# Kernel optimization log

Measured on AMD Instinct MI355X. Metric: run time of the kernel, lower is better.

The kernel has to match this reference:

```python
import jax, jax.numpy as jnp
import numpy as np
import math

L, E, H, F, V, ML, B, S = 6, 1024, 16, 4096, 1024, 1024, 4, 1024
PAD = V - 1


def setup_inputs() -> dict:
    key = jax.random.key(0)
    ks = jax.random.split(key, 16)
    sc = 0.02
    nrm = lambda k, sh: jax.random.normal(k, sh, jnp.float32) * sc
    return dict(
        sequences=jax.random.randint(ks[0], (B, S), 0, V - 1),
        embed=nrm(ks[1], (V, E)),
        pos_emb=nrm(ks[2], (1, ML + 2, E)),
        dist_emb=nrm(ks[3], (ML + 1, H)),
        in_w=nrm(ks[4], (L, 3 * E, E)), in_b=nrm(ks[5], (L, 3 * E)),
        out_w=nrm(ks[6], (L, E, E)), out_b=nrm(ks[7], (L, E)),
        ln1_g=jnp.ones((L, E)), ln1_b=jnp.zeros((L, E)),
        ff1_w=nrm(ks[8], (L, F, E)), ff1_b=nrm(ks[9], (L, F)),
        ff2_w=nrm(ks[10], (L, E, F)), ff2_b=nrm(ks[11], (L, E)),
        ln2_g=jnp.ones((L, E)), ln2_b=jnp.zeros((L, E)),
        lnf_g=jnp.ones((E,)), lnf_b=jnp.zeros((E,)),
        gen_w=nrm(ks[12], (V, E)), gen_b=jnp.zeros((V,)),
    )


def _layer_norm(h, g, b, eps=1e-5):
    m = h.mean(-1, keepdims=True)
    v = ((h - m) ** 2).mean(-1, keepdims=True)
    return (h - m) * jax.lax.rsqrt(v + eps) * g + b


def reference(sequences, embed, pos_emb, dist_emb, in_w, in_b, out_w, out_b,
              ln1_g, ln1_b, ff1_w, ff1_b, ff2_w, ff2_b, ln2_g, ln2_b,
              lnf_g, lnf_b, gen_w, gen_b):
    b_, s_ = sequences.shape
    dh = E // H
    # token embedding * sqrt(E) + learned positional embedding
    x = embed[sequences] * math.sqrt(E) + pos_emb[:, :s_]  # [B,S,E]
    # relative-distance attention bias, clamped at max_len
    idx = jnp.arange(s_)
    dist = jnp.minimum(jnp.abs(idx[None, :] - idx[:, None]), ML)  # [S,S]
    bias = dist_emb[dist].transpose(2, 0, 1)[None]  # [1,H,S,S]
    causal = idx[None, :] <= idx[:, None]  # lower-triangular allowed
    bias = jnp.where(causal[None, None], bias, -jnp.inf)
    # key padding mask (additive -inf on padded keys)
    kpm = (sequences == PAD)  # [B,S]
    bias = jnp.where(kpm[:, None, None, :], -jnp.inf, bias)  # [B,H,S,S]

    scale = 1.0 / math.sqrt(dh)
    for l in range(L):
        qkv = jnp.einsum('bse,fe->bsf', x, in_w[l]) + in_b[l]
        q, k, v = jnp.split(qkv, 3, axis=-1)
        q = q.reshape(b_, s_, H, dh).transpose(0, 2, 1, 3)
        k = k.reshape(b_, s_, H, dh).transpose(0, 2, 1, 3)
        v = v.reshape(b_, s_, H, dh).transpose(0, 2, 1, 3)
        scores = jnp.einsum('bhqd,bhkd->bhqk', q, k) * scale + bias
        att = jax.nn.softmax(scores, axis=-1)
        ctx = jnp.einsum('bhqk,bhkd->bhqd', att, v)
        ctx = ctx.transpose(0, 2, 1, 3).reshape(b_, s_, E)
        attn_out = jnp.einsum('bse,fe->bsf', ctx, out_w[l]) + out_b[l]
        x = _layer_norm(x + attn_out, ln1_g[l], ln1_b[l])  # post-norm
        h = jax.nn.gelu(jnp.einsum('bse,fe->bsf', x, ff1_w[l]) + ff1_b[l], approximate=False)
        h = jnp.einsum('bsf,ef->bse', h, ff2_w[l]) + ff2_b[l]
        x = _layer_norm(x + h, ln2_g[l], ln2_b[l])
    x = _layer_norm(x, lnf_g, lnf_b)  # final encoder norm
    logits = jnp.einsum('bse,ve->bsv', x, gen_w) + gen_b
    return logits
```

## Files before the change

### kernel.cpp

```cpp
#include <hip/hip_runtime.h>
#include <math.h>
#include <stdint.h>

constexpr int kL = 6;
constexpr int kE = 1024;
constexpr int kH = 16;
constexpr int kF = 4096;
constexpr int kV = 1024;
constexpr int kB = 4;
constexpr int kS = 1024;
constexpr int kRows = kB * kS;

typedef __bf16 bf16_t;
typedef __bf16 bf16x8 __attribute__((ext_vector_type(8)));
typedef __bf16 bf16x4 __attribute__((ext_vector_type(4)));
typedef float f32x4 __attribute__((ext_vector_type(4)));
typedef unsigned int u32x2 __attribute__((ext_vector_type(2)));

#define AS1 __attribute__((address_space(1)))
#define AS3 __attribute__((address_space(3)))

__device__ __forceinline__ void gload_lds16(const void* g, void* l) {
  __builtin_amdgcn_global_load_lds((const AS1 unsigned int*)g, (AS3 unsigned int*)l, 16, 0, 0);
}

__device__ __forceinline__ unsigned lds_u32(const void* p) {
  return (unsigned)(uintptr_t)p;
}

__device__ __forceinline__ float gelu_f(float x) {
  return 0.5f * x * (1.0f + erff(x * 0.70710678118654752440f));
}

template <int CTRL>
__device__ __forceinline__ float dppf(float v) {
  return __builtin_bit_cast(float, __builtin_amdgcn_update_dpp(
      __builtin_bit_cast(int, v), __builtin_bit_cast(int, v), CTRL, 0xF, 0xF, false));
}

__global__ void cast_kernel(const float* __restrict__ in, bf16_t* __restrict__ out, int n4) {
  const int stride = gridDim.x * blockDim.x;
  for (int i = blockIdx.x * blockDim.x + threadIdx.x; i < n4; i += stride) {
    const float4 v = *(const float4*)(in + (size_t)i * 4);
    bf16x4 o;
    o[0] = (bf16_t)v.x; o[1] = (bf16_t)v.y; o[2] = (bf16_t)v.z; o[3] = (bf16_t)v.w;
    *(bf16x4*)(out + (size_t)i * 4) = o;
  }
}

__global__ void embed_kernel(const int* __restrict__ seq, const float* __restrict__ emb,
                             const float* __restrict__ pos, float* __restrict__ x32,
                             bf16_t* __restrict__ xb) {
  const int r = blockIdx.x;
  const int s = r & 1023;
  const int tok = seq[r];
  const int c = threadIdx.x << 2;
  const float4 e = *(const float4*)(emb + (size_t)tok * kE + c);
  const float4 pz = *(const float4*)(pos + (size_t)s * kE + c);
  float4 v;
  v.x = e.x * 32.0f + pz.x;
  v.y = e.y * 32.0f + pz.y;
  v.z = e.z * 32.0f + pz.z;
  v.w = e.w * 32.0f + pz.w;
  *(float4*)(x32 + (size_t)r * kE + c) = v;
  bf16x4 o;
  o[0] = (bf16_t)v.x; o[1] = (bf16_t)v.y; o[2] = (bf16_t)v.z; o[3] = (bf16_t)v.w;
  *(bf16x4*)(xb + (size_t)r * kE + c) = o;
}

template <int MODE>
__global__ void addln_kernel(float* __restrict__ x32, const void* __restrict__ res,
                             const float* __restrict__ gg, const float* __restrict__ bb,
                             bf16_t* __restrict__ xb, const float* __restrict__ bias2) {
  __shared__ float red[8];
  const int r = blockIdx.x;
  const int c = threadIdx.x << 2;
  float4 v = *(const float4*)(x32 + (size_t)r * kE + c);
  if (MODE == 0) {
    const bf16x4 t = *(const bf16x4*)((const bf16_t*)res + (size_t)r * kE + c);
    v.x += (float)t[0]; v.y += (float)t[1]; v.z += (float)t[2]; v.w += (float)t[3];
  }
  if (MODE == 2) {
    const bf16_t* p = (const bf16_t*)res;
#pragma unroll
    for (int part = 0; part < 4; ++part) {
      const bf16x4 t = *(const bf16x4*)(p + (size_t)part * kRows * kE + (size_t)r * kE + c);
      v.x += (float)t[0]; v.y += (float)t[1]; v.z += (float)t[2]; v.w += (float)t[3];
    }
    const float4 b2 = *(const float4*)(bias2 + c);
    v.x += b2.x; v.y += b2.y; v.z += b2.z; v.w += b2.w;
  }
  float s = v.x + v.y + v.z + v.w;
  float q = v.x * v.x + v.y * v.y + v.z * v.z + v.w * v.w;
#pragma unroll
  for (int off = 32; off >= 1; off >>= 1) {
    s += __shfl_xor(s, off, 64);
    q += __shfl_xor(q, off, 64);
  }
  const int w = threadIdx.x >> 6, lane = threadIdx.x & 63;
  if (lane == 0) { red[w] = s; red[4 + w] = q; }
  __syncthreads();
  s = red[0] + red[1] + red[2] + red[3];
  q = red[4] + red[5] + red[6] + red[7];
  const float mean = s * (1.0f / 1024.0f);
  const float var = q * (1.0f / 1024.0f) - mean * mean;
  const float rstd = rsqrtf(var + 1e-5f);
  const float4 g4 = *(const float4*)(gg + c);
  const float4 b4 = *(const float4*)(bb + c);
  float4 o;
  o.x = (v.x - mean) * rstd * g4.x + b4.x;
  o.y = (v.y - mean) * rstd * g4.y + b4.y;
  o.z = (v.z - mean) * rstd * g4.z + b4.z;
  o.w = (v.w - mean) * rstd * g4.w + b4.w;
  if (MODE != 1) *(float4*)(x32 + (size_t)r * kE + c) = o;
  bf16x4 ob;
  ob[0] = (bf16_t)o.x; ob[1] = (bf16_t)o.y; ob[2] = (bf16_t)o.z; ob[3] = (bf16_t)o.w;
  *(bf16x4*)(xb + (size_t)r * kE + c) = ob;
}

template <int EPI>
__launch_bounds__(256, 3)
__global__ void gemm_bt_kernel(const bf16_t* __restrict__ A, const bf16_t* __restrict__ Bt,
                               const float* __restrict__ bias, void* __restrict__ Cv,
                               int M, int N, int K) {
  __shared__ bf16_t lA[128 * 32];
  __shared__ bf16_t lB[128 * 32];
  const int tid = threadIdx.x;
  const int w = tid >> 6;
  const int lane = tid & 63;
  const int g = lane >> 4;
  const int lr = lane & 15;
  const int bm0 = blockIdx.y << 7;
  const int bn0 = blockIdx.x << 7;
  const int wm = (w >> 1) << 6;
  const int wn = (w & 1) << 6;

  const int sr = lane >> 2;
  const int sc = (lane & 3) << 4;

  const char* srcA0 = (const char*)(A + (size_t)(bm0 + (w << 5) + sr) * K) + sc;
  const char* srcA1 = (const char*)(A + (size_t)(bm0 + (w << 5) + 16 + sr) * K) + sc;
  const char* srcB0 = (const char*)(Bt + (size_t)(bn0 + (w << 5) + sr) * K) + sc;
  const char* srcB1 = (const char*)(Bt + (size_t)(bn0 + (w << 5) + 16 + sr) * K) + sc;
  bf16_t* dA0 = lA + (size_t)(w << 5) * 32;
  bf16_t* dA1 = lA + (size_t)((w << 5) + 16) * 32;
  bf16_t* dB0 = lB + (size_t)(w << 5) * 32;
  bf16_t* dB1 = lB + (size_t)((w << 5) + 16) * 32;

  f32x4 zz = {0.f, 0.f, 0.f, 0.f};
  f32x4 acc[4][4];
#pragma unroll
  for (int i = 0; i < 4; ++i)
#pragma unroll
    for (int j = 0; j < 4; ++j) acc[i][j] = zz;

  const bf16_t* pa[4];
  const bf16_t* pb[4];
#pragma unroll
  for (int i = 0; i < 4; ++i) {
    pa[i] = lA + (size_t)(wm + i * 16 + lr) * 32 + g * 8;
    pb[i] = lB + (size_t)(wn + i * 16 + lr) * 32 + g * 8;
  }

  const int NT = K >> 5;
  for (int t = 0; t < NT; ++t) {
    gload_lds16(srcA0, dA0);
    gload_lds16(srcA1, dA1);
    gload_lds16(srcB0, dB0);
    gload_lds16(srcB1, dB1);
    srcA0 += 64; srcA1 += 64; srcB0 += 64; srcB1 += 64;
    __syncthreads();
    bf16x8 a[4], b[4];
#pragma unroll
    for (int i = 0; i < 4; ++i) a[i] = *(const bf16x8*)pa[i];
#pragma unroll
    for (int i = 0; i < 4; ++i) b[i] = *(const bf16x8*)pb[i];
#pragma unroll
    for (int i = 0; i < 4; ++i)
#pragma unroll
      for (int j = 0; j < 4; ++j)
        acc[i][j] = __builtin_amdgcn_mfma_f32_16x16x32_bf16(a[i], b[j], acc[i][j], 0, 0, 0);
    __syncthreads();
  }

#pragma unroll
  for (int i = 0; i < 4; ++i) {
#pragma unroll
    for (int j = 0; j < 4; ++j) {
      const int col = bn0 + wn + j * 16 + lr;
      const float bv = bias[col];
#pragma unroll
      for (int rg = 0; rg < 4; ++rg) {
        const int row = bm0 + wm + i * 16 + g * 4 + rg;
        float v = acc[i][j][rg] + bv;
        if (EPI == 1) {
          ((float*)Cv)[(size_t)row * N + col] = v;
        } else {
          ((bf16_t*)Cv)[(size_t)row * N + col] = (bf16_t)v;
        }
      }
    }
  }
}

template <int EPI>
__launch_bounds__(512, 2)
__global__ void gemm256_kernel(const bf16_t* __restrict__ A, const bf16_t* __restrict__ Bt,
                               const float* __restrict__ bias, void* __restrict__ Cv,
                               int ldA, int ldB, int ldC, int kc, size_t zstride) {
  __shared__ bf16_t lA[2][256 * 64];
  __shared__ bf16_t lB[2][256 * 64];
  const int tid = threadIdx.x;
  const int w = tid >> 6, lane = tid & 63, g = lane >> 4, lr = lane & 15;

  const int nwg = gridDim.x * gridDim.y;
  const int lin = blockIdx.y * gridDim.x + blockIdx.x;
  const int cpx = nwg >> 3;
  const int swz = (lin & 7) * cpx + (lin >> 3);
  const int bx = swz % gridDim.x, by = swz / gridDim.x;
  const int bm0 = by << 8, bn0 = bx << 8;
  const int wr = w >> 2, wc = w & 3;
  const int wm = wr << 7, wn = wc << 6;
  const int k0 = blockIdx.z * kc;

  const int lrow = lane >> 3, lcol8 = lane & 7;
  const int scol = ((lcol8 ^ lrow) << 3);
  const bf16_t* pA = A + (size_t)(bm0 + lrow) * ldA + k0 + scol;
  const bf16_t* pB = Bt + (size_t)(bn0 + lrow) * ldB + k0 + scol;

  const int ra1_0 = w * 8,                        ra1_1 = 128 + w * 8;
  const int ra4_0 = 64 + w * 8,                   ra4_1 = 192 + w * 8;
  const int rb2_0 = (w >> 2) * 64 + (w & 3) * 8,  rb2_1 = rb2_0 + 128;
  const int rb3_0 = rb2_0 + 32,                   rb3_1 = rb2_1 + 32;

#define STG_A(bufi, t, rb) gload_lds16(pA + (size_t)(rb) * ldA + (t) * 64, &lA[bufi][(rb) * 64])
#define STG_B(bufi, t, rb) gload_lds16(pB + (size_t)(rb) * ldB + (t) * 64, &lB[bufi][(rb) * 64])
#define STAGE_R1(bufi, t) { STG_A(bufi, t, ra1_0); STG_A(bufi, t, ra1_1); }
#define STAGE_R2(bufi, t) { STG_B(bufi, t, rb2_0); STG_B(bufi, t, rb2_1); }
#define STAGE_R3(bufi, t) { STG_B(bufi, t, rb3_0); STG_B(bufi, t, rb3_1); }
#define STAGE_R4(bufi, t) { STG_A(bufi, t, ra4_0); STG_A(bufi, t, ra4_1); }

  const int cs0 = (g * 8) ^ ((lr & 7) << 3);
  const int cs1 = (32 + g * 8) ^ ((lr & 7) << 3);
#define LDA8(bufi, row, cs) (*(const bf16x8*)&lA[bufi][(row) * 64 + (cs)])
#define LDB8(bufi, row, cs) (*(const bf16x8*)&lB[bufi][(row) * 64 + (cs)])

#define PH_MID()                                          \
  __builtin_amdgcn_sched_barrier(0);                      \
  __builtin_amdgcn_s_barrier();                           \
  asm volatile("s_waitcnt lgkmcnt(0)" ::: "memory");      \
  __builtin_amdgcn_sched_barrier(0);                      \
  __builtin_amdgcn_s_setprio(1)

#define PH_END()                                          \
  __builtin_amdgcn_s_setprio(0);                          \
  __builtin_amdgcn_sched_barrier(0);                      \
  __builtin_amdgcn_s_barrier();                           \
  __builtin_amdgcn_sched_barrier(0)

#define PH_END_VM()                                       \
  __builtin_amdgcn_s_setprio(0);                          \
  __builtin_amdgcn_sched_barrier(0);                      \
  asm volatile("s_waitcnt vmcnt(6)" ::: "memory");        \
  __builtin_amdgcn_s_barrier();                           \
  __builtin_amdgcn_sched_barrier(0)

  f32x4 zz = {0.f, 0.f, 0.f, 0.f};
  f32x4 acc[8][4];
#pragma unroll
  for (int i = 0; i < 8; ++i)
#pragma unroll
    for (int j = 0; j < 4; ++j) acc[i][j] = zz;

  const int NT = kc >> 6;

  STAGE_R1(0, 0); STAGE_R2(0, 0); STAGE_R3(0, 0); STAGE_R4(0, 0);
  STAGE_R1(1, 1); STAGE_R2(1, 1); STAGE_R3(1, 1);
  asm volatile("s_waitcnt vmcnt(6)" ::: "memory");
  __builtin_amdgcn_s_barrier();
  __builtin_amdgcn_sched_barrier(0);

  bf16x8 a0[4][2], a1[4][2], b[4][2];

  for (int t = 0; t < NT; ++t) {
    const int bz = t & 1;
#pragma unroll
    for (int i = 0; i < 4; ++i) {
      a0[i][0] = LDA8(bz, wm + i * 16 + lr, cs0);
      a0[i][1] = LDA8(bz, wm + i * 16 + lr, cs1);
    }
#pragma unroll
    for (int j = 0; j < 2; ++j) {
      b[j][0] = LDB8(bz, wn + j * 16 + lr, cs0);
      b[j][1] = LDB8(bz, wn + j * 16 + lr, cs1);
    }
    if (t + 1 < NT) STAGE_R4(bz ^ 1, t + 1);
    PH_MID();
#pragma unroll
    for (int i = 0; i < 4; ++i)
#pragma unroll
      for (int j = 0; j < 2; ++j) {
        acc[i][j] = __builtin_amdgcn_mfma_f32_16x16x32_bf16(a0[i][0], b[j][0], acc[i][j], 0, 0, 0);
        acc[i][j] = __builtin_amdgcn_mfma_f32_16x16x32_bf16(a0[i][1], b[j][1], acc[i][j], 0, 0, 0);
      }
    PH_END();
#pragma unroll
    for (int j = 2; j < 4; ++j) {
      b[j][0] = LDB8(bz, wn + j * 16 + lr, cs0);
      b[j][1] = LDB8(bz, wn + j * 16 + lr, cs1);
    }
    if (t + 2 < NT) STAGE_R1(bz, t + 2);
    PH_MID();
#pragma unroll
    for (int i = 0; i < 4; ++i)
#pragma unroll
      for (int j = 2; j < 4; ++j) {
        acc[i][j] = __builtin_amdgcn_mfma_f32_16x16x32_bf16(a0[i][0], b[j][0], acc[i][j], 0, 0, 0);
        acc[i][j] = __builtin_amdgcn_mfma_f32_16x16x32_bf16(a0[i][1], b[j][1], acc[i][j], 0, 0, 0);
      }
    PH_END();
#pragma unroll
    for (int i = 0; i < 4; ++i) {
      a1[i][0] = LDA8(bz, wm + 64 + i * 16 + lr, cs0);
      a1[i][1] = LDA8(bz, wm + 64 + i * 16 + lr, cs1);
    }
    if (t + 2 < NT) STAGE_R2(bz, t + 2);
    PH_MID();
#pragma unroll
    for (int i = 0; i < 4; ++i)
#pragma unroll
      for (int j = 0; j < 2; ++j) {
        acc[4 + i][j] = __builtin_amdgcn_mfma_f32_16x16x32_bf16(a1[i][0], b[j][0], acc[4 + i][j], 0, 0, 0);
        acc[4 + i][j] = __builtin_amdgcn_mfma_f32_16x16x32_bf16(a1[i][1], b[j][1], acc[4 + i][j], 0, 0, 0);
      }
    PH_END();
    if (t + 2 < NT) STAGE_R3(bz, t + 2);
    PH_MID();
#pragma unroll
    for (int i = 0; i < 4; ++i)
#pragma unroll
      for (int j = 2; j < 4; ++j) {
        acc[4 + i][j] = __builtin_amdgcn_mfma_f32_16x16x32_bf16(a1[i][0], b[j][0], acc[4 + i][j], 0, 0, 0);
        acc[4 + i][j] = __builtin_amdgcn_mfma_f32_16x16x32_bf16(a1[i][1], b[j][1], acc[4 + i][j], 0, 0, 0);
      }
    PH_END_VM();
  }

  bf16_t* outb = (bf16_t*)Cv;
  if (EPI == 3) outb += (size_t)blockIdx.z * zstride;
#pragma unroll
  for (int i = 0; i < 8; ++i) {
#pragma unroll
    for (int j = 0; j < 4; ++j) {
      const int col = bn0 + wn + j * 16 + lr;
      float bv = 0.0f;
      if (EPI != 3) bv = bias[col];
#pragma unroll
      for (int rg = 0; rg < 4; ++rg) {
        const int row = bm0 + wm + i * 16 + g * 4 + rg;
        float v = acc[i][j][rg] + bv;
        if (EPI == 2) v = gelu_f(v);
        outb[(size_t)row * ldC + col] = (bf16_t)v;
      }
    }
  }
#undef STG_A
#undef STG_B
#undef STAGE_R1
#undef STAGE_R2
#undef STAGE_R3
#undef STAGE_R4
#undef LDA8
#undef LDB8
#undef PH_MID
#undef PH_END
#undef PH_END_VM
}

__launch_bounds__(256, 3)
__global__ void attn_kernel(const bf16_t* __restrict__ qkv, const int* __restrict__ seq,
                            const float* __restrict__ dist_emb, bf16_t* __restrict__ ctx) {
  __shared__ float sbias[1024];
  __shared__ unsigned char spad[1024];
  __shared__ bf16_t kbuf[2][64 * 64];
  __shared__ bf16_t vbuf[2][4096];
  __shared__ bf16_t pbuf[4][16][72];
  const int tid = threadIdx.x;
  const int w = tid >> 6, lane = tid & 63, g = lane >> 4, lr = lane & 15;
  const int bid = blockIdx.x;
  const int qt = 15 - (bid >> 6);
  const int h = bid & 15, b = (bid >> 4) & 3;

  const int q0 = qt * 64 + w * 16;
  const bf16_t* qp = qkv + ((size_t)(b * kS + q0 + lr)) * 3072 + h * 64;

  const int p = (w * 64 + lane) * 16;
  const int s_kv = ((p >> 11) << 4) + ((p >> 5) & 15);
  const int s_dv = (((p >> 9) & 3) << 4) + ((p & 31) >> 1);
  const bf16_t* vsrc0 = qkv + ((size_t)(b * kS + s_kv)) * 3072 + 2048 + h * 64 + s_dv;

  const int klrow = (w << 3) + (lane >> 3);
  const int kscol = ((lane & 7) ^ (lane >> 3)) << 3;
  const bf16_t* ksrc0 = qkv + ((size_t)(b * kS + klrow)) * 3072 + 1024 + h * 64 + kscol;

  const int cs0k = (g ^ (lr & 7)) << 3;
  const int cs1k = ((4 + g) ^ (lr & 7)) << 3;

  const int* seqb = seq + b * kS;
  const int nt = qt + 1;

#define STAGEKV(bufi, kt_) {                                                        \
    gload_lds16(ksrc0 + (size_t)((kt_) * 64) * 3072, &kbuf[bufi][(w << 3) * 64]);   \
    gload_lds16(ksrc0 + (size_t)((kt_) * 64 + 32) * 3072,                           \
                &kbuf[bufi][(32 + (w << 3)) * 64]);                                 \
    gload_lds16(vsrc0 + (size_t)((kt_) * 64) * 3072, &vbuf[bufi][w << 9]);          \
    gload_lds16(vsrc0 + (size_t)((kt_) * 64 + 32) * 3072,                           \
                &vbuf[bufi][2048 + (w << 9)]);                                      \
  }

  STAGEKV(0, 0);
  const bf16x8 qf0 = *(const bf16x8*)(qp + g * 8);
  const bf16x8 qf1 = *(const bf16x8*)(qp + 32 + g * 8);
  for (int i = tid; i < 1024; i += 256) {
    sbias[i] = dist_emb[i * kH + h];
    spad[i] = (seqb[i] == kV - 1) ? 1 : 0;
  }

  f32x4 zz = {0.f, 0.f, 0.f, 0.f};
  f32x4 oacc[4];
#pragma unroll
  for (int n = 0; n < 4; ++n) oacc[n] = zz;
  float m_[4], l_[4];
#pragma unroll
  for (int j = 0; j < 4; ++j) { m_[j] = -1e30f; l_[j] = 0.f; }

  __syncthreads();

#define ATT_STEP64(kt_, bz) do {                                                    \
    bf16x8 kf0[4], kf1[4];                                                          \
    _Pragma("unroll")                                                               \
    for (int ns = 0; ns < 4; ++ns) {                                                \
      const int krow = (ns * 16 + lr) * 64;                                         \
      kf0[ns] = *(const bf16x8*)&kbuf[bz][krow + cs0k];                             \
      kf1[ns] = *(const bf16x8*)&kbuf[bz][krow + cs1k];                             \
    }                                                                               \
    f32x4 s_[4];                                                                    \
    _Pragma("unroll")                                                               \
    for (int ns = 0; ns < 4; ++ns) {                                                \
      f32x4 z = zz;                                                                 \
      z = __builtin_amdgcn_mfma_f32_16x16x32_bf16(qf0, kf0[ns], z, 0, 0, 0);        \
      z = __builtin_amdgcn_mfma_f32_16x16x32_bf16(qf1, kf1[ns], z, 0, 0, 0);        \
      s_[ns] = z;                                                                   \
    }                                                                               \
    const int colb = (kt_) * 64 + lr;                                               \
    bool pad[4];                                                                    \
    _Pragma("unroll")                                                               \
    for (int ns = 0; ns < 4; ++ns) pad[ns] = spad[colb + ns * 16] != 0;             \
    float sv[4][4], mj[4];                                                          \
    _Pragma("unroll")                                                               \
    for (int j = 0; j < 4; ++j) {                                                   \
      const int r = q0 + g * 4 + j;                                                 \
      _Pragma("unroll")                                                             \
      for (int ns = 0; ns < 4; ++ns) {                                              \
        const int cc = colb + ns * 16;                                              \
        sv[ns][j] = (cc <= r && !pad[ns]) ? s_[ns][j] * 0.125f + sbias[r - cc]      \
                                          : -1e30f;                                 \
      }                                                                             \
      mj[j] = fmaxf(fmaxf(sv[0][j], sv[1][j]), fmaxf(sv[2][j], sv[3][j]));          \
      mj[j] = fmaxf(mj[j], dppf<0x121>(mj[j]));                                     \
      mj[j] = fmaxf(mj[j], dppf<0x122>(mj[j]));                                     \
      mj[j] = fmaxf(mj[j], dppf<0x124>(mj[j]));                                     \
      mj[j] = fmaxf(mj[j], dppf<0x128>(mj[j]));                                     \
    }                                                                               \
    float corr[4], pv[4][4];                                                        \
    _Pragma("unroll")                                                               \
    for (int j = 0; j < 4; ++j) {                                                   \
      const float mn = fmaxf(m_[j], mj[j]);                                         \
      corr[j] = __expf(m_[j] - mn);                                                 \
      m_[j] = mn;                                                                   \
      _Pragma("unroll")                                                             \
      for (int ns = 0; ns < 4; ++ns) pv[ns][j] = __expf(sv[ns][j] - mn);            \
      float rs = (pv[0][j] + pv[1][j]) + (pv[2][j] + pv[3][j]);                     \
      rs += dppf<0x121>(rs);                                                        \
      rs += dppf<0x122>(rs);                                                        \
      rs += dppf<0x124>(rs);                                                        \
      rs += dppf<0x128>(rs);                                                        \
      l_[j] = l_[j] * corr[j] + rs;                                                 \
    }                                                                               \
    _Pragma("unroll")                                                               \
    for (int n = 0; n < 4; ++n) {                                                   \
      f32x4 t = oacc[n];                                                            \
      t[0] *= corr[0]; t[1] *= corr[1]; t[2] *= corr[2]; t[3] *= corr[3];           \
      oacc[n] = t;                                                                  \
    }                                                                               \
    _Pragma("unroll")                                                               \
    for (int j = 0; j < 4; ++j) {                                                   \
      _Pragma("unroll")                                                             \
      for (int ns = 0; ns < 4; ++ns)                                                \
        pbuf[w][g * 4 + j][ns * 16 + lr] = (bf16_t)pv[ns][j];                       \
    }                                                                               \
    asm volatile("s_waitcnt lgkmcnt(0)" ::: "memory");                              \
    const bf16x4 pa0 = *(const bf16x4*)&pbuf[w][lr][g * 4];                         \
    const bf16x4 pa1 = *(const bf16x4*)&pbuf[w][lr][16 + g * 4];                    \
    const bf16x4 pa2 = *(const bf16x4*)&pbuf[w][lr][32 + g * 4];                    \
    const bf16x4 pa3 = *(const bf16x4*)&pbuf[w][lr][48 + g * 4];                    \
    bf16x8 pfl, pfh;                                                                \
    _Pragma("unroll")                                                               \
    for (int j = 0; j < 4; ++j) {                                                   \
      pfl[j] = pa0[j]; pfl[4 + j] = pa1[j];                                         \
      pfh[j] = pa2[j]; pfh[4 + j] = pa3[j];                                         \
    }                                                                               \
    const unsigned vb0 = lds_u32(&vbuf[bz][0]) + g * 128 + lr * 8;                  \
    u32x2 vt[8], vth[8];                                                            \
    _Pragma("unroll")                                                               \
    for (int n = 0; n < 4; ++n) {                                                   \
      asm volatile("ds_read_b64_tr_b16 %0, %2\n\t"                                  \
                   "ds_read_b64_tr_b16 %1, %2 offset:2048"                          \
                   : "=&v"(vt[n * 2]), "=&v"(vt[n * 2 + 1])                         \
                   : "v"(vb0 + n * 512)                                             \
                   : "memory");                                                     \
      asm volatile("ds_read_b64_tr_b16 %0, %2 offset:4096\n\t"                      \
                   "ds_read_b64_tr_b16 %1, %2 offset:6144"                          \
                   : "=&v"(vth[n * 2]), "=&v"(vth[n * 2 + 1])                       \
                   : "v"(vb0 + n * 512)                                             \
                   : "memory");                                                     \
    }                                                                               \
    asm volatile("s_waitcnt lgkmcnt(0)" ::: "memory");                              \
    __builtin_amdgcn_sched_barrier(0);                                              \
    _Pragma("unroll")                                                               \
    for (int n = 0; n < 4; ++n) {                                                   \
      const bf16x4 v0 = __builtin_bit_cast(bf16x4, vt[n * 2]);                      \
      const bf16x4 v1 = __builtin_bit_cast(bf16x4, vt[n * 2 + 1]);                  \
      bf16x8 vf;                                                                    \
      _Pragma("unroll")                                                             \
      for (int j = 0; j < 4; ++j) { vf[j] = v0[j]; vf[4 + j] = v1[j]; }             \
      oacc[n] = __builtin_amdgcn_mfma_f32_16x16x32_bf16(pfl, vf, oacc[n], 0, 0, 0); \
      const bf16x4 h0 = __builtin_bit_cast(bf16x4, vth[n * 2]);                     \
      const bf16x4 h1 = __builtin_bit_cast(bf16x4, vth[n * 2 + 1]);                 \
      bf16x8 vfh;                                                                   \
      _Pragma("unroll")                                                             \
      for (int j = 0; j < 4; ++j) { vfh[j] = h0[j]; vfh[4 + j] = h1[j]; }           \
      oacc[n] = __builtin_amdgcn_mfma_f32_16x16x32_bf16(pfh, vfh, oacc[n], 0, 0, 0);\
    }                                                                               \
  } while (0)

  for (int kt = 0; kt < nt; kt += 2) {
    if (kt + 1 < nt) STAGEKV(1, kt + 1);
    ATT_STEP64(kt, 0);
    __syncthreads();
    if (kt + 2 < nt) STAGEKV(0, kt + 2);
    if (kt + 1 < nt) ATT_STEP64(kt + 1, 1);
    __syncthreads();
  }
#undef ATT_STEP64
#undef STAGEKV

#pragma unroll
  for (int j = 0; j < 4; ++j) {
    const float inv = 1.0f / l_[j];
    const int r = q0 + g * 4 + j;
    bf16_t* dst = ctx + ((size_t)(b * kS + r)) * kE + h * 64;
#pragma unroll
    for (int n = 0; n < 4; ++n) dst[n * 16 + lr] = (bf16_t)(oacc[n][j] * inv);
  }
}

extern "C" void kernel_launch(void* const* d_in, const int* in_sizes, int n_in,
                              void* d_out, int out_size, void* d_ws, size_t ws_size,
                              hipStream_t stream) {
  (void)in_sizes; (void)n_in; (void)out_size;
  const int* seq = (const int*)d_in[0];
  const float* emb = (const float*)d_in[1];
  const float* pos = (const float*)d_in[2];
  const float* dist = (const float*)d_in[3];
  const float* in_w = (const float*)d_in[4];
  const float* in_b = (const float*)d_in[5];
  const float* out_w = (const float*)d_in[6];
  const float* out_b = (const float*)d_in[7];
  const float* ln1g = (const float*)d_in[8];
  const float* ln1b = (const float*)d_in[9];
  const float* ff1w = (const float*)d_in[10];
  const float* ff1b = (const float*)d_in[11];
  const float* ff2w = (const float*)d_in[12];
  const float* ff2b = (const float*)d_in[13];
  const float* ln2g = (const float*)d_in[14];
  const float* ln2b = (const float*)d_in[15];
  const float* lnfg = (const float*)d_in[16];
  const float* lnfb = (const float*)d_in[17];
  const float* genw = (const float*)d_in[18];
  const float* genb = (const float*)d_in[19];

  char* ws = (char*)d_ws;
  size_t off = 0;
  auto alloc = [&](size_t elems, size_t esz) -> void* {
    void* pp = ws + off;
    off += (elems * esz + 255) & ~(size_t)255;
    return pp;
  };
  bf16_t* w_in = (bf16_t*)alloc((size_t)kL * 3 * kE * kE, 2);
  bf16_t* w_out = (bf16_t*)alloc((size_t)kL * kE * kE, 2);
  bf16_t* w_f1 = (bf16_t*)alloc((size_t)kL * kF * kE, 2);
  bf16_t* w_f2 = (bf16_t*)alloc((size_t)kL * kE * kF, 2);
  bf16_t* w_g = (bf16_t*)alloc((size_t)kV * kE, 2);
  float* x32 = (float*)alloc((size_t)kRows * kE, 4);
  bf16_t* xb = (bf16_t*)alloc((size_t)kRows * kE, 2);
  bf16_t* qkvb = (bf16_t*)alloc((size_t)kRows * 3 * kE, 2);
  bf16_t* ctxb = (bf16_t*)alloc((size_t)kRows * kE, 2);
  bf16_t* tmp4 = (bf16_t*)alloc((size_t)4 * kRows * kE, 2);
  bf16_t* hb = (bf16_t*)alloc((size_t)kRows * kF, 2);
  if (off > ws_size) return;

  cast_kernel<<<2048, 256, 0, stream>>>(in_w, w_in, kL * 3 * kE * kE / 4);
  cast_kernel<<<2048, 256, 0, stream>>>(out_w, w_out, kL * kE * kE / 4);
  cast_kernel<<<2048, 256, 0, stream>>>(ff1w, w_f1, kL * kF * kE / 4);
  cast_kernel<<<2048, 256, 0, stream>>>(ff2w, w_f2, kL * kE * kF / 4);
  cast_kernel<<<1024, 256, 0, stream>>>(genw, w_g, kV * kE / 4);
  embed_kernel<<<kRows, 256, 0, stream>>>(seq, emb, pos, x32, xb);

  for (int l = 0; l < kL; ++l) {
    gemm256_kernel<0><<<dim3(3 * kE / 256, kRows / 256), 512, 0, stream>>>(
        xb, w_in + (size_t)l * 3 * kE * kE, in_b + (size_t)l * 3 * kE, qkvb,
        kE, kE, 3 * kE, kE, 0);
    attn_kernel<<<kB * kH * 16, 256, 0, stream>>>(qkvb, seq, dist, ctxb);
    gemm256_kernel<3><<<dim3(kE / 256, kRows / 256, 4), 512, 0, stream>>>(
        ctxb, w_out + (size_t)l * kE * kE, nullptr, tmp4,
        kE, kE, kE, 256, (size_t)kRows * kE);
    addln_kernel<2><<<kRows, 256, 0, stream>>>(x32, tmp4, ln1g + (size_t)l * kE,
                                               ln1b + (size_t)l * kE, xb, out_b + (size_t)l * kE);
    gemm256_kernel<2><<<dim3(kF / 256, kRows / 256), 512, 0, stream>>>(
        xb, w_f1 + (size_t)l * kF * kE, ff1b + (size_t)l * kF, hb,
        kE, kE, kF, kE, 0);
    gemm256_kernel<3><<<dim3(kE / 256, kRows / 256, 4), 512, 0, stream>>>(
        hb, w_f2 + (size_t)l * kE * kF, nullptr, tmp4,
        kF, kF, kE, kE, (size_t)kRows * kE);
    addln_kernel<2><<<kRows, 256, 0, stream>>>(x32, tmp4, ln2g + (size_t)l * kE,
                                               ln2b + (size_t)l * kE, xb, ff2b + (size_t)l * kE);
  }
  addln_kernel<1><<<kRows, 256, 0, stream>>>(x32, nullptr, lnfg, lnfb, xb, nullptr);
  gemm_bt_kernel<1><<<dim3(kV / 128, kRows / 128), 256, 0, stream>>>(
      xb, w_g, genb, (float*)d_out, kRows, kV, kE);
}
```

Measured before the change: 1.417 ms.

## Replace 256x256 pipelined GEMM with generalized 128x128 GEMM kernel

Removes the large 256x256 tile GEMM with double-buffered LDS and phased MFMA/load scheduling. All projection and FFN GEMMs now use the simpler 128x128 tile kernel, which gains leading-dimension, K-split and grid-swizzle parameters. This gives more workgroups and smaller LDS use, in exchange for less data reuse per tile and no overlap of loads with compute inside a workgroup.

```diff
diff --git a/kernel.cpp b/kernel.cpp
--- a/kernel.cpp
+++ b/kernel.cpp
@@ -120,9 +120,9 @@
 
 template <int EPI>
 __launch_bounds__(256, 3)
-__global__ void gemm_bt_kernel(const bf16_t* __restrict__ A, const bf16_t* __restrict__ Bt,
+__global__ void gemm128_kernel(const bf16_t* __restrict__ A, const bf16_t* __restrict__ Bt,
                                const float* __restrict__ bias, void* __restrict__ Cv,
-                               int M, int N, int K) {
+                               int ldA, int ldB, int ldC, int kc, size_t zstride) {
   __shared__ bf16_t lA[128 * 32];
   __shared__ bf16_t lB[128 * 32];
   const int tid = threadIdx.x;
@@ -130,18 +130,25 @@
   const int lane = tid & 63;
   const int g = lane >> 4;
   const int lr = lane & 15;
-  const int bm0 = blockIdx.y << 7;
-  const int bn0 = blockIdx.x << 7;
+
+  const int nwg = gridDim.x * gridDim.y;
+  const int lin = blockIdx.y * gridDim.x + blockIdx.x;
+  const int cpx = nwg >> 3;
+  const int swz = (lin & 7) * cpx + (lin >> 3);
+  const int bx = swz % gridDim.x, by = swz / gridDim.x;
+  const int bm0 = by << 7;
+  const int bn0 = bx << 7;
+  const int k0 = blockIdx.z * kc;
   const int wm = (w >> 1) << 6;
   const int wn = (w & 1) << 6;
 
   const int sr = lane >> 2;
   const int sc = (lane & 3) << 4;
 
-  const char* srcA0 = (const char*)(A + (size_t)(bm0 + (w << 5) + sr) * K) + sc;
-  const char* srcA1 = (const char*)(A + (size_t)(bm0 + (w << 5) + 16 + sr) * K) + sc;
-  const char* srcB0 = (const char*)(Bt + (size_t)(bn0 + (w << 5) + sr) * K) + sc;
-  const char* srcB1 = (const char*)(Bt + (size_t)(bn0 + (w << 5) + 16 + sr) * K) + sc;
+  const char* srcA0 = (const char*)(A + (size_t)(bm0 + (w << 5) + sr) * ldA + k0) + sc;
+  const char* srcA1 = (const char*)(A + (size_t)(bm0 + (w << 5) + 16 + sr) * ldA + k0) + sc;
+  const char* srcB0 = (const char*)(Bt + (size_t)(bn0 + (w << 5) + sr) * ldB + k0) + sc;
+  const char* srcB1 = (const char*)(Bt + (size_t)(bn0 + (w << 5) + 16 + sr) * ldB + k0) + sc;
   bf16_t* dA0 = lA + (size_t)(w << 5) * 32;
   bf16_t* dA1 = lA + (size_t)((w << 5) + 16) * 32;
   bf16_t* dB0 = lB + (size_t)(w << 5) * 32;
@@ -162,7 +169,7 @@
     pb[i] = lB + (size_t)(wn + i * 16 + lr) * 32 + g * 8;
   }
 
-  const int NT = K >> 5;
+  const int NT = kc >> 5;
   for (int t = 0; t < NT; ++t) {
     gload_lds16(srcA0, dA0);
     gload_lds16(srcA1, dA1);
@@ -183,173 +190,10 @@
     __syncthreads();
   }
 
-#pragma unroll
-  for (int i = 0; i < 4; ++i) {
-#pragma unroll
-    for (int j = 0; j < 4; ++j) {
-      const int col = bn0 + wn + j * 16 + lr;
-      const float bv = bias[col];
-#pragma unroll
-      for (int rg = 0; rg < 4; ++rg) {
-        const int row = bm0 + wm + i * 16 + g * 4 + rg;
-        float v = acc[i][j][rg] + bv;
-        if (EPI == 1) {
-          ((float*)Cv)[(size_t)row * N + col] = v;
-        } else {
-          ((bf16_t*)Cv)[(size_t)row * N + col] = (bf16_t)v;
-        }
-      }
-    }
-  }
-}
-
-template <int EPI>
-__launch_bounds__(512, 2)
-__global__ void gemm256_kernel(const bf16_t* __restrict__ A, const bf16_t* __restrict__ Bt,
-                               const float* __restrict__ bias, void* __restrict__ Cv,
-                               int ldA, int ldB, int ldC, int kc, size_t zstride) {
-  __shared__ bf16_t lA[2][256 * 64];
-  __shared__ bf16_t lB[2][256 * 64];
-  const int tid = threadIdx.x;
-  const int w = tid >> 6, lane = tid & 63, g = lane >> 4, lr = lane & 15;
-
-  const int nwg = gridDim.x * gridDim.y;
-  const int lin = blockIdx.y * gridDim.x + blockIdx.x;
-  const int cpx = nwg >> 3;
-  const int swz = (lin & 7) * cpx + (lin >> 3);
-  const int bx = swz % gridDim.x, by = swz / gridDim.x;
-  const int bm0 = by << 8, bn0 = bx << 8;
-  const int wr = w >> 2, wc = w & 3;
-  const int wm = wr << 7, wn = wc << 6;
-  const int k0 = blockIdx.z * kc;
-
-  const int lrow = lane >> 3, lcol8 = lane & 7;
-  const int scol = ((lcol8 ^ lrow) << 3);
-  const bf16_t* pA = A + (size_t)(bm0 + lrow) * ldA + k0 + scol;
-  const bf16_t* pB = Bt + (size_t)(bn0 + lrow) * ldB + k0 + scol;
-
-  const int ra1_0 = w * 8,                        ra1_1 = 128 + w * 8;
-  const int ra4_0 = 64 + w * 8,                   ra4_1 = 192 + w * 8;
-  const int rb2_0 = (w >> 2) * 64 + (w & 3) * 8,  rb2_1 = rb2_0 + 128;
-  const int rb3_0 = rb2_0 + 32,                   rb3_1 = rb2_1 + 32;
-
-#define STG_A(bufi, t, rb) gload_lds16(pA + (size_t)(rb) * ldA + (t) * 64, &lA[bufi][(rb) * 64])
-#define STG_B(bufi, t, rb) gload_lds16(pB + (size_t)(rb) * ldB + (t) * 64, &lB[bufi][(rb) * 64])
-#define STAGE_R1(bufi, t) { STG_A(bufi, t, ra1_0); STG_A(bufi, t, ra1_1); }
-#define STAGE_R2(bufi, t) { STG_B(bufi, t, rb2_0); STG_B(bufi, t, rb2_1); }
-#define STAGE_R3(bufi, t) { STG_B(bufi, t, rb3_0); STG_B(bufi, t, rb3_1); }
-#define STAGE_R4(bufi, t) { STG_A(bufi, t, ra4_0); STG_A(bufi, t, ra4_1); }
-
-  const int cs0 = (g * 8) ^ ((lr & 7) << 3);
-  const int cs1 = (32 + g * 8) ^ ((lr & 7) << 3);
-#define LDA8(bufi, row, cs) (*(const bf16x8*)&lA[bufi][(row) * 64 + (cs)])
-#define LDB8(bufi, row, cs) (*(const bf16x8*)&lB[bufi][(row) * 64 + (cs)])
-
-#define PH_MID()                                          \
-  __builtin_amdgcn_sched_barrier(0);                      \
-  __builtin_amdgcn_s_barrier();                           \
-  asm volatile("s_waitcnt lgkmcnt(0)" ::: "memory");      \
-  __builtin_amdgcn_sched_barrier(0);                      \
-  __builtin_amdgcn_s_setprio(1)
-
-#define PH_END()                                          \
-  __builtin_amdgcn_s_setprio(0);                          \
-  __builtin_amdgcn_sched_barrier(0);                      \
-  __builtin_amdgcn_s_barrier();                           \
-  __builtin_amdgcn_sched_barrier(0)
-
-#define PH_END_VM()                                       \
-  __builtin_amdgcn_s_setprio(0);                          \
-  __builtin_amdgcn_sched_barrier(0);                      \
-  asm volatile("s_waitcnt vmcnt(6)" ::: "memory");        \
-  __builtin_amdgcn_s_barrier();                           \
-  __builtin_amdgcn_sched_barrier(0)
-
-  f32x4 zz = {0.f, 0.f, 0.f, 0.f};
-  f32x4 acc[8][4];
-#pragma unroll
-  for (int i = 0; i < 8; ++i)
-#pragma unroll
-    for (int j = 0; j < 4; ++j) acc[i][j] = zz;
-
-  const int NT = kc >> 6;
-
-  STAGE_R1(0, 0); STAGE_R2(0, 0); STAGE_R3(0, 0); STAGE_R4(0, 0);
-  STAGE_R1(1, 1); STAGE_R2(1, 1); STAGE_R3(1, 1);
-  asm volatile("s_waitcnt vmcnt(6)" ::: "memory");
-  __builtin_amdgcn_s_barrier();
-  __builtin_amdgcn_sched_barrier(0);
-
-  bf16x8 a0[4][2], a1[4][2], b[4][2];
-
-  for (int t = 0; t < NT; ++t) {
-    const int bz = t & 1;
-#pragma unroll
-    for (int i = 0; i < 4; ++i) {
-      a0[i][0] = LDA8(bz, wm + i * 16 + lr, cs0);
-      a0[i][1] = LDA8(bz, wm + i * 16 + lr, cs1);
-    }
-#pragma unroll
-    for (int j = 0; j < 2; ++j) {
-      b[j][0] = LDB8(bz, wn + j * 16 + lr, cs0);
-      b[j][1] = LDB8(bz, wn + j * 16 + lr, cs1);
-    }
-    if (t + 1 < NT) STAGE_R4(bz ^ 1, t + 1);
-    PH_MID();
-#pragma unroll
-    for (int i = 0; i < 4; ++i)
-#pragma unroll
-      for (int j = 0; j < 2; ++j) {
-        acc[i][j] = __builtin_amdgcn_mfma_f32_16x16x32_bf16(a0[i][0], b[j][0], acc[i][j], 0, 0, 0);
-        acc[i][j] = __builtin_amdgcn_mfma_f32_16x16x32_bf16(a0[i][1], b[j][1], acc[i][j], 0, 0, 0);
-      }
-    PH_END();
-#pragma unroll
-    for (int j = 2; j < 4; ++j) {
-      b[j][0] = LDB8(bz, wn + j * 16 + lr, cs0);
-      b[j][1] = LDB8(bz, wn + j * 16 + lr, cs1);
-    }
-    if (t + 2 < NT) STAGE_R1(bz, t + 2);
-    PH_MID();
-#pragma unroll
-    for (int i = 0; i < 4; ++i)
-#pragma unroll
-      for (int j = 2; j < 4; ++j) {
-        acc[i][j] = __builtin_amdgcn_mfma_f32_16x16x32_bf16(a0[i][0], b[j][0], acc[i][j], 0, 0, 0);
-        acc[i][j] = __builtin_amdgcn_mfma_f32_16x16x32_bf16(a0[i][1], b[j][1], acc[i][j], 0, 0, 0);
-      }
-    PH_END();
-#pragma unroll
-    for (int i = 0; i < 4; ++i) {
-      a1[i][0] = LDA8(bz, wm + 64 + i * 16 + lr, cs0);
-      a1[i][1] = LDA8(bz, wm + 64 + i * 16 + lr, cs1);
-    }
-    if (t + 2 < NT) STAGE_R2(bz, t + 2);
-    PH_MID();
-#pragma unroll
-    for (int i = 0; i < 4; ++i)
-#pragma unroll
-      for (int j = 0; j < 2; ++j) {
-        acc[4 + i][j] = __builtin_amdgcn_mfma_f32_16x16x32_bf16(a1[i][0], b[j][0], acc[4 + i][j], 0, 0, 0);
-        acc[4 + i][j] = __builtin_amdgcn_mfma_f32_16x16x32_bf16(a1[i][1], b[j][1], acc[4 + i][j], 0, 0, 0);
-      }
-    PH_END();
-    if (t + 2 < NT) STAGE_R3(bz, t + 2);
-    PH_MID();
-#pragma unroll
-    for (int i = 0; i < 4; ++i)
-#pragma unroll
-      for (int j = 2; j < 4; ++j) {
-        acc[4 + i][j] = __builtin_amdgcn_mfma_f32_16x16x32_bf16(a1[i][0], b[j][0], acc[4 + i][j], 0, 0, 0);
-        acc[4 + i][j] = __builtin_amdgcn_mfma_f32_16x16x32_bf16(a1[i][1], b[j][1], acc[4 + i][j], 0, 0, 0);
-      }
-    PH_END_VM();
-  }
-
   bf16_t* outb = (bf16_t*)Cv;
   if (EPI == 3) outb += (size_t)blockIdx.z * zstride;
 #pragma unroll
-  for (int i = 0; i < 8; ++i) {
+  for (int i = 0; i < 4; ++i) {
 #pragma unroll
     for (int j = 0; j < 4; ++j) {
       const int col = bn0 + wn + j * 16 + lr;
@@ -360,21 +204,14 @@
         const int row = bm0 + wm + i * 16 + g * 4 + rg;
         float v = acc[i][j][rg] + bv;
         if (EPI == 2) v = gelu_f(v);
-        outb[(size_t)row * ldC + col] = (bf16_t)v;
+        if (EPI == 1) {
+          ((float*)Cv)[(size_t)row * ldC + col] = v;
+        } else {
+          outb[(size_t)row * ldC + col] = (bf16_t)v;
+        }
       }
     }
   }
-#undef STG_A
-#undef STG_B
-#undef STAGE_R1
-#undef STAGE_R2
-#undef STAGE_R3
-#undef STAGE_R4
-#undef LDA8
-#undef LDB8
-#undef PH_MID
-#undef PH_END
-#undef PH_END_VM
 }
 
 __launch_bounds__(256, 3)
@@ -618,25 +455,25 @@
   embed_kernel<<<kRows, 256, 0, stream>>>(seq, emb, pos, x32, xb);
 
   for (int l = 0; l < kL; ++l) {
-    gemm256_kernel<0><<<dim3(3 * kE / 256, kRows / 256), 512, 0, stream>>>(
+    gemm128_kernel<0><<<dim3(3 * kE / 128, kRows / 128), 256, 0, stream>>>(
         xb, w_in + (size_t)l * 3 * kE * kE, in_b + (size_t)l * 3 * kE, qkvb,
         kE, kE, 3 * kE, kE, 0);
     attn_kernel<<<kB * kH * 16, 256, 0, stream>>>(qkvb, seq, dist, ctxb);
-    gemm256_kernel<3><<<dim3(kE / 256, kRows / 256, 4), 512, 0, stream>>>(
+    gemm128_kernel<3><<<dim3(kE / 128, kRows / 128, 4), 256, 0, stream>>>(
         ctxb, w_out + (size_t)l * kE * kE, nullptr, tmp4,
         kE, kE, kE, 256, (size_t)kRows * kE);
     addln_kernel<2><<<kRows, 256, 0, stream>>>(x32, tmp4, ln1g + (size_t)l * kE,
                                                ln1b + (size_t)l * kE, xb, out_b + (size_t)l * kE);
-    gemm256_kernel<2><<<dim3(kF / 256, kRows / 256), 512, 0, stream>>>(
+    gemm128_kernel<2><<<dim3(kF / 128, kRows / 128), 256, 0, stream>>>(
         xb, w_f1 + (size_t)l * kF * kE, ff1b + (size_t)l * kF, hb,
         kE, kE, kF, kE, 0);
-    gemm256_kernel<3><<<dim3(kE / 256, kRows / 256, 4), 512, 0, stream>>>(
+    gemm128_kernel<3><<<dim3(kE / 128, kRows / 128, 4), 256, 0, stream>>>(
         hb, w_f2 + (size_t)l * kE * kF, nullptr, tmp4,
         kF, kF, kE, kE, (size_t)kRows * kE);
     addln_kernel<2><<<kRows, 256, 0, stream>>>(x32, tmp4, ln2g + (size_t)l * kE,
                                                ln2b + (size_t)l * kE, xb, ff2b + (size_t)l * kE);
   }
   addln_kernel<1><<<kRows, 256, 0, stream>>>(x32, nullptr, lnfg, lnfb, xb, nullptr);
-  gemm_bt_kernel<1><<<dim3(kV / 128, kRows / 128), 256, 0, stream>>>(
-      xb, w_g, genb, (float*)d_out, kRows, kV, kE);
-}
+  gemm128_kernel<1><<<dim3(kV / 128, kRows / 128), 256, 0, stream>>>(
+      xb, w_g, genb, (float*)d_out, kE, kE, kV, kE, 0);
+}
```

Result: no change. 1.413 ms (-0.3%).
